# Kernel tuning notes

Hardware: AMD Instinct MI355X
Metric: run time of the kernel (lower is better)

Reference implementation:

```python
import jax, jax.numpy as jnp
import numpy as np

B, IN_C, NHEAD, ATT_C, OUT_C, H, W = 512, 256, 8, 32, 32, 19, 19
EPS = 1e-5


def setup_inputs() -> dict:
    key = jax.random.key(0)
    ks = jax.random.split(key, 4)
    f32 = jnp.float32
    return {
        "x": jax.random.normal(ks[0], (B, IN_C, H, W), f32),
        "Wq": jax.random.normal(ks[1], (NHEAD * ATT_C, IN_C), f32) * 0.05,
        "bq": jnp.zeros((NHEAD * ATT_C,), f32),
        "Wk": jax.random.normal(ks[2], (NHEAD * ATT_C, IN_C), f32) * 0.05,
        "bk": jnp.zeros((NHEAD * ATT_C,), f32),
        "Wv": jax.random.normal(ks[3], (NHEAD * OUT_C, IN_C), f32) * 0.05,
        "bv": jnp.zeros((NHEAD * OUT_C,), f32),
        "gQ": jnp.ones((NHEAD * ATT_C,), f32),
        "betaQ": jnp.zeros((NHEAD * ATT_C,), f32),
        "gK": jnp.ones((NHEAD * ATT_C,), f32),
        "betaK": jnp.zeros((NHEAD * ATT_C,), f32),
        "gV": jnp.ones((NHEAD * OUT_C,), f32),
        "betaV": jnp.zeros((NHEAD * OUT_C,), f32),
    }


def _conv1x1(x, Wt, bt):
    # x: [B,Ci,H,W], Wt: [Co,Ci] -> [B,Co,H,W]
    return jnp.einsum("oi,bihw->bohw", Wt, x) + bt[None, :, None, None]


def _bn(x, g, b):
    # training-mode BatchNorm2d: batch stats over (N,H,W)
    mu = x.mean(axis=(0, 2, 3), keepdims=True)
    var = x.var(axis=(0, 2, 3), keepdims=True)
    return (x - mu) * jax.lax.rsqrt(var + EPS) * g[None, :, None, None] + b[None, :, None, None]


def _neighbors(t):
    # t: [B,C,H,W] -> [B,4,C,H,W] zero-padded 4-neighbor shifts (up,down,left,right)
    p = jnp.pad(t, ((0, 0), (0, 0), (1, 1), (1, 1)))
    return jnp.stack(
        (p[:, :, 0:-2, 1:-1], p[:, :, 2:, 1:-1], p[:, :, 1:-1, 0:-2], p[:, :, 1:-1, 2:]),
        axis=1,
    )


def reference(x, Wq, bq, Wk, bk, Wv, bv, gQ, betaQ, gK, betaK, gV, betaV):
    Q = _bn(_conv1x1(x, Wq, bq), gQ, betaQ)
    K = _bn(_conv1x1(x, Wk, bk), gK, betaK)
    V = _bn(_conv1x1(x, Wv, bv), gV, betaV)

    Kn = _neighbors(K).reshape(B, 4, NHEAD, ATT_C, H, W)
    Q4 = Q.reshape(B, 1, NHEAD, ATT_C, H, W)
    # attention logits: mean over att_c, then * sqrt(att_c)  (usenormmean == 0)
    a = (Q4 * Kn).mean(axis=3) * jnp.float32(ATT_C ** 0.5)  # [B,4,nhead,H,W]
    a = jax.nn.softmax(a, axis=1)[:, :, :, None]  # [B,4,nhead,1,H,W]

    Vn = _neighbors(V).reshape(B, 4, NHEAD, OUT_C, H, W)
    out = (a * Vn).sum(axis=1)  # [B,nhead,out_c,H,W]
    out = out.reshape(B, NHEAD * OUT_C, H, W)
    out = jax.nn.relu(out)  # useRelu == 1
    return out + x  # residual
```

## Files before the change

### kernel.cpp

```cpp
#include <hip/hip_runtime.h>

typedef unsigned short u16;
typedef unsigned int   u32;

#define NB     512
#define NHEADS 8
#define HW     361
#define NPIX   184832
#define NTOT   768
#define EPSBN  1e-5f
#define RS     0.17677669529663687f
#define PSTR   104

typedef __bf16 bf16x8 __attribute__((ext_vector_type(8)));
typedef float  f32x4  __attribute__((ext_vector_type(4)));

__device__ __forceinline__ u16 f2bf(float f) {
  u32 u = __float_as_uint(f);
  u += 0x7fffu + ((u >> 16) & 1u);
  return (u16)(u >> 16);
}
__device__ __forceinline__ float bf2f(u16 v) {
  return __uint_as_float(((u32)v) << 16);
}
__device__ __forceinline__ bf16x8 ldb8(const void* p) {
  return __builtin_bit_cast(bf16x8, *(const uint4*)p);
}
__device__ __forceinline__ float dot2(u32 a, u32 b) {
  return bf2f((u16)a) * bf2f((u16)b) + bf2f((u16)(a >> 16)) * bf2f((u16)(b >> 16));
}
__device__ __forceinline__ float dot8(uint4 a, uint4 b) {
  return dot2(a.x, b.x) + dot2(a.y, b.y) + dot2(a.z, b.z) + dot2(a.w, b.w);
}

__global__ __launch_bounds__(256) void k_prep(
    const float* __restrict__ Wq, const float* __restrict__ bq,
    const float* __restrict__ Wk, const float* __restrict__ bk,
    const float* __restrict__ Wv, const float* __restrict__ bv,
    u16* __restrict__ Wall, float* __restrict__ ball,
    float* __restrict__ sx) {
  const int n = blockIdx.x, t = threadIdx.x;
  const float* src; const float* bs; int r;
  if (n < 256)      { src = Wq; bs = bq; r = n; }
  else if (n < 512) { src = Wk; bs = bk; r = n - 256; }
  else              { src = Wv; bs = bv; r = n - 512; }
  Wall[n * 256 + t] = f2bf(src[r * 256 + t]);
  if (t == 0) ball[n] = bs[r];
  if (n == 0) sx[t] = 0.f;
}

__global__ __launch_bounds__(512) void k_M(
    const float* __restrict__ x, u16* __restrict__ xT,
    float* __restrict__ Mpart, float* __restrict__ sx) {
  __shared__ u16 Als[256 * 64];
  const int tid = threadIdx.x, g = blockIdx.x;
  const int lane = tid & 63, w = tid >> 6;
  const int l15 = lane & 15, kq = lane >> 4;
  const int sc  = tid >> 4;
  const int sq  = tid & 15;
  const int wpx = tid & 63;
  const int wcs = tid >> 6;
  char* Ab = (char*)Als;

  float sxp[8];
  f32x4 acc[2][16];
  #pragma unroll
  for (int i = 0; i < 8; ++i) sxp[i] = 0.f;
  #pragma unroll
  for (int f2 = 0; f2 < 16; ++f2) {
    acc[0][f2] = (f32x4){0.f, 0.f, 0.f, 0.f};
    acc[1][f2] = (f32x4){0.f, 0.f, 0.f, 0.f};
  }

  #pragma unroll 1
  for (int ch = 0; ch < 12; ++ch) {
    const int img = (ch >= 6) ? 1 : 0;
    const int px0 = (ch - img * 6) * 64;
    const int bb  = g * 2 + img;
    const int pb  = px0 + sq * 4;
    #pragma unroll
    for (int i = 0; i < 8; ++i) {
      const int c = sc + 32 * i;
      const float* xp = x + ((size_t)bb * 256 + c) * HW + pb;
      float v0, v1, v2, v3;
      if (pb + 3 < HW) {
        const float4 f4 = *(const float4*)xp;
        v0 = f4.x; v1 = f4.y; v2 = f4.z; v3 = f4.w;
      } else {
        v0 = (pb + 0 < HW) ? xp[0] : 0.f;
        v1 = (pb + 1 < HW) ? xp[1] : 0.f;
        v2 = (pb + 2 < HW) ? xp[2] : 0.f;
        v3 = (pb + 3 < HW) ? xp[3] : 0.f;
      }
      sxp[i] += v0 + v1 + v2 + v3;
      const u32 lo = (u32)f2bf(v0) | ((u32)f2bf(v1) << 16);
      const u32 hi = (u32)f2bf(v2) | ((u32)f2bf(v3) << 16);
      const int slot = (sq >> 1) ^ (c & 7);
      *(uint2*)(Ab + c * 128 + slot * 16 + (sq & 1) * 8) = make_uint2(lo, hi);
    }
    __syncthreads();
    #pragma unroll
    for (int kk = 0; kk < 2; ++kk) {
      const int gl = kk * 4 + kq;
      const int so = ((gl ^ (l15 & 7)) << 4);
      const int r0 = w * 32 + l15;
      const bf16x8 a0 = ldb8(Ab + r0 * 128 + so);
      const bf16x8 a1 = ldb8(Ab + (r0 + 16) * 128 + so);
      #pragma unroll
      for (int f2 = 0; f2 < 16; ++f2) {
        const bf16x8 b = ldb8(Ab + (f2 * 16 + l15) * 128 + so);
        acc[0][f2] = __builtin_amdgcn_mfma_f32_16x16x32_bf16(a0, b, acc[0][f2], 0, 0, 0);
        acc[1][f2] = __builtin_amdgcn_mfma_f32_16x16x32_bf16(a1, b, acc[1][f2], 0, 0, 0);
      }
    }
    const int pxg = px0 + wpx;
    if (pxg < HW) {
      __align__(16) u16 tmp[32];
      #pragma unroll
      for (int j = 0; j < 32; ++j) {
        const int c = wcs * 32 + j;
        tmp[j] = Als[c * 64 + (((wpx >> 3) ^ (c & 7)) << 3) + (wpx & 7)];
      }
      uint4* dst = (uint4*)(xT + ((size_t)bb * HW + pxg) * 256 + wcs * 32);
      dst[0] = ((const uint4*)tmp)[0];
      dst[1] = ((const uint4*)tmp)[1];
      dst[2] = ((const uint4*)tmp)[2];
      dst[3] = ((const uint4*)tmp)[3];
    }
    __syncthreads();
  }
  float* mp = Mpart + (size_t)g * 65536;
  #pragma unroll
  for (int f1 = 0; f1 < 2; ++f1)
    #pragma unroll
    for (int f2 = 0; f2 < 16; ++f2)
      #pragma unroll
      for (int j = 0; j < 4; ++j) {
        const int c1 = w * 32 + f1 * 16 + kq * 4 + j;
        const int c2 = f2 * 16 + l15;
        mp[c1 * 256 + c2] = acc[f1][f2][j];
      }
  #pragma unroll
  for (int i = 0; i < 8; ++i) {
    float v = sxp[i];
    v += __shfl_down(v, 8); v += __shfl_down(v, 4);
    v += __shfl_down(v, 2); v += __shfl_down(v, 1);
    if (sq == 0) atomicAdd(&sx[sc + 32 * i], v);
  }
}

__global__ __launch_bounds__(256) void k_red(const float* __restrict__ Mpart,
                                             float* __restrict__ Mg) {
  const int i = blockIdx.x * 256 + threadIdx.x;
  float s = 0.f;
  #pragma unroll 8
  for (int sl = 0; sl < 256; ++sl) s += Mpart[(size_t)sl * 65536 + i];
  Mg[i] = s;
}

__global__ __launch_bounds__(256) void k_stats2(
    const float* __restrict__ Mg, const float* __restrict__ sx,
    const float* __restrict__ Wq, const float* __restrict__ bq,
    const float* __restrict__ Wk, const float* __restrict__ bk,
    const float* __restrict__ Wv, const float* __restrict__ bv,
    const float* __restrict__ gQ, const float* __restrict__ betaQ,
    const float* __restrict__ gK, const float* __restrict__ betaK,
    const float* __restrict__ gV, const float* __restrict__ betaV,
    float* __restrict__ s_all, float* __restrict__ t_all) {
  __shared__ float ws[256];
  __shared__ float r1[4], r2[4];
  const int n = blockIdx.x, i = threadIdx.x;
  const int which = n >> 8, r = n & 255;
  const float* src = (which == 0) ? Wq : (which == 1) ? Wk : Wv;
  const float wi = src[r * 256 + i];
  ws[i] = wi;
  __syncthreads();
  float colsum = 0.f;
  #pragma unroll 4
  for (int j = 0; j < 256; ++j) colsum += Mg[j * 256 + i] * ws[j];
  float p1 = wi * sx[i];
  float p2 = wi * colsum;
  p1 += __shfl_down(p1, 32); p2 += __shfl_down(p2, 32);
  p1 += __shfl_down(p1, 16); p2 += __shfl_down(p2, 16);
  p1 += __shfl_down(p1, 8);  p2 += __shfl_down(p2, 8);
  p1 += __shfl_down(p1, 4);  p2 += __shfl_down(p2, 4);
  p1 += __shfl_down(p1, 2);  p2 += __shfl_down(p2, 2);
  p1 += __shfl_down(p1, 1);  p2 += __shfl_down(p2, 1);
  const int wv = i >> 6;
  if ((i & 63) == 0) { r1[wv] = p1; r2[wv] = p2; }
  __syncthreads();
  if (i == 0) {
    const float S1 = r1[0] + r1[1] + r1[2] + r1[3];
    const float S2 = r2[0] + r2[1] + r2[2] + r2[3];
    const float* bs = (which == 0) ? bq : (which == 1) ? bk : bv;
    const float* gs = (which == 0) ? gQ : (which == 1) ? gK : gV;
    const float* be = (which == 0) ? betaQ : (which == 1) ? betaK : betaV;
    const float b = bs[r];
    const float P = (float)NPIX;
    const float mean = (S1 + P * b) / P;
    const float Ey2  = (S2 + 2.f * b * S1 + P * b * b) / P;
    const float var  = Ey2 - mean * mean;
    const float s    = gs[r] * rsqrtf(var + EPSBN);
    s_all[n] = s;
    t_all[n] = be[r] - s * mean;
  }
}

__global__ __launch_bounds__(768) void k_fused(
    const u16* __restrict__ xT, const u16* __restrict__ Wall,
    const float* __restrict__ ball,
    const float* __restrict__ s_all, const float* __restrict__ t_all,
    const float* __restrict__ x, float* __restrict__ out) {
  __shared__ u16   Wl[96 * 256];
  __shared__ __align__(16) u16 P[HW * PSTR];
  __shared__ float aL[4 * HW];
  __shared__ float stl[2 * 96];
  const int tid = threadIdx.x;
  const int wg  = blockIdx.x;
  const int bb  = (wg & 7) + 8 * (wg >> 6);
  const int h   = (wg >> 3) & 7;
  const char* Pb = (const char*)P;

  const bool pact = tid < 2 * HW;
  const int  ppx  = pact ? ((tid < HW) ? tid : tid - HW) : 0;
  const int  poc0 = (tid < HW) ? 0 : 16;
  const size_t pgb = ((size_t)bb * 256 + h * 32 + poc0) * HW + ppx;
  float xres[16];
  if (pact) {
    #pragma unroll
    for (int o = 0; o < 16; ++o) xres[o] = x[pgb + (size_t)o * HW];
  }

  if (tid < 96) {
    const int which = tid >> 5, c32 = tid & 31;
    const int n = which * 256 + h * 32 + c32;
    float s = s_all[n];
    float t = s * ball[n] + t_all[n];
    if (tid < 32) { s *= RS; t *= RS; }
    stl[tid] = s; stl[96 + tid] = t;
  }
  #pragma unroll
  for (int i = 0; i < 4; ++i) {
    const int gi = tid + i * 768;
    const int lr = gi >> 5, gg = gi & 31;
    const int which = lr >> 5, c32 = lr & 31;
    uint4 v = *(const uint4*)(Wall + (size_t)(which * 256 + h * 32 + c32) * 256 + gg * 8);
    const int slot = gg ^ (lr & 7);
    *(uint4*)((char*)Wl + lr * 512 + slot * 16) = v;
  }
  __syncthreads();

  const int lane = tid & 63, wv = tid >> 6;
  const int l15 = lane & 15, kq = lane >> 4;
  const u16* xTb = xT + (size_t)bb * HW * 256;

  uint4 bfr[16];
  #pragma unroll
  for (int ks = 0; ks < 8; ++ks) {
    bfr[2 * ks]     = *(const uint4*)(xTb + (size_t)(wv * 32      + l15) * 256 + ks * 32 + kq * 8);
    bfr[2 * ks + 1] = *(const uint4*)(xTb + (size_t)(wv * 32 + 16 + l15) * 256 + ks * 32 + kq * 8);
  }

  f32x4 acc[6][2];
  #pragma unroll
  for (int f = 0; f < 6; ++f) { acc[f][0] = (f32x4){0.f,0.f,0.f,0.f}; acc[f][1] = (f32x4){0.f,0.f,0.f,0.f}; }

  #pragma unroll
  for (int ks = 0; ks < 8; ++ks) {
    bf16x8 b0 = __builtin_bit_cast(bf16x8, bfr[2 * ks]);
    bf16x8 b1 = __builtin_bit_cast(bf16x8, bfr[2 * ks + 1]);
    const int slot = ((ks * 4 + kq) ^ (l15 & 7)) * 16;
    #pragma unroll
    for (int f = 0; f < 6; ++f) {
      const int lr = (f >> 1) * 32 + (f & 1) * 16 + l15;
      bf16x8 a = ldb8((const char*)Wl + lr * 512 + slot);
      acc[f][0] = __builtin_amdgcn_mfma_f32_16x16x32_bf16(a, b0, acc[f][0], 0, 0, 0);
      acc[f][1] = __builtin_amdgcn_mfma_f32_16x16x32_bf16(a, b1, acc[f][1], 0, 0, 0);
    }
  }
  #pragma unroll
  for (int f = 0; f < 6; ++f) {
    #pragma unroll
    for (int j = 0; j < 4; ++j) {
      const int ch = f * 16 + kq * 4 + j;
      const float s = stl[ch], t = stl[96 + ch];
      #pragma unroll
      for (int p2 = 0; p2 < 2; ++p2) {
        const int px = wv * 32 + p2 * 16 + l15;
        if (px < HW) P[px * PSTR + ch] = f2bf(s * acc[f][p2][j] + t);
      }
    }
  }
  __syncthreads();

  if (tid < HW) {
    const int px = tid;
    const int yy = px / 19, xx = px - yy * 19;
    const bool i0 = yy > 0, i1 = yy < 18, i2 = xx > 0, i3 = xx < 18;
    const int pn0 = i0 ? px - 19 : px, pn1 = i1 ? px + 19 : px;
    const int pn2 = i2 ? px - 1  : px, pn3 = i3 ? px + 1  : px;
    const uint4* Qp = (const uint4*)(Pb + px * 208);
    const uint4 q0 = Qp[0], q1 = Qp[1], q2 = Qp[2], q3 = Qp[3];
    const uint4* K0 = (const uint4*)(Pb + pn0 * 208 + 64);
    const uint4* K1 = (const uint4*)(Pb + pn1 * 208 + 64);
    const uint4* K2 = (const uint4*)(Pb + pn2 * 208 + 64);
    const uint4* K3 = (const uint4*)(Pb + pn3 * 208 + 64);
    float l0 = dot8(q0, K0[0]) + dot8(q1, K0[1]) + dot8(q2, K0[2]) + dot8(q3, K0[3]);
    float l1 = dot8(q0, K1[0]) + dot8(q1, K1[1]) + dot8(q2, K1[2]) + dot8(q3, K1[3]);
    float l2 = dot8(q0, K2[0]) + dot8(q1, K2[1]) + dot8(q2, K2[2]) + dot8(q3, K2[3]);
    float l3 = dot8(q0, K3[0]) + dot8(q1, K3[1]) + dot8(q2, K3[2]) + dot8(q3, K3[3]);
    l0 = i0 ? l0 : 0.f; l1 = i1 ? l1 : 0.f;
    l2 = i2 ? l2 : 0.f; l3 = i3 ? l3 : 0.f;
    const float mx = fmaxf(fmaxf(l0, l1), fmaxf(l2, l3));
    const float e0 = __expf(l0 - mx), e1 = __expf(l1 - mx);
    const float e2 = __expf(l2 - mx), e3 = __expf(l3 - mx);
    const float inv = 1.f / (e0 + e1 + e2 + e3);
    aL[0 * HW + px] = i0 ? e0 * inv : 0.f;
    aL[1 * HW + px] = i1 ? e1 * inv : 0.f;
    aL[2 * HW + px] = i2 ? e2 * inv : 0.f;
    aL[3 * HW + px] = i3 ? e3 * inv : 0.f;
  }
  __syncthreads();

  if (pact) {
    const int px = ppx;
    const int yy = px / 19, xx = px - yy * 19;
    const int pn0 = (yy > 0)  ? px - 19 : px, pn1 = (yy < 18) ? px + 19 : px;
    const int pn2 = (xx > 0)  ? px - 1  : px, pn3 = (xx < 18) ? px + 1  : px;
    const float a0 = aL[0 * HW + px], a1 = aL[1 * HW + px];
    const float a2 = aL[2 * HW + px], a3 = aL[3 * HW + px];
    const int vb = 128 + poc0 * 2;
    const uint4* V0 = (const uint4*)(Pb + pn0 * 208 + vb);
    const uint4* V1 = (const uint4*)(Pb + pn1 * 208 + vb);
    const uint4* V2 = (const uint4*)(Pb + pn2 * 208 + vb);
    const uint4* V3 = (const uint4*)(Pb + pn3 * 208 + vb);
    #pragma unroll
    for (int half = 0; half < 2; ++half) {
      const uint4 w0 = V0[half], w1 = V1[half], w2 = V2[half], w3 = V3[half];
      const u32 u0[4] = {w0.x, w0.y, w0.z, w0.w};
      const u32 u1[4] = {w1.x, w1.y, w1.z, w1.w};
      const u32 u2[4] = {w2.x, w2.y, w2.z, w2.w};
      const u32 u3[4] = {w3.x, w3.y, w3.z, w3.w};
      #pragma unroll
      for (int p = 0; p < 4; ++p) {
        const int o = half * 8 + p * 2;
        float vlo = a0 * bf2f((u16)u0[p]) + a1 * bf2f((u16)u1[p])
                  + a2 * bf2f((u16)u2[p]) + a3 * bf2f((u16)u3[p]);
        float vhi = a0 * bf2f((u16)(u0[p] >> 16)) + a1 * bf2f((u16)(u1[p] >> 16))
                  + a2 * bf2f((u16)(u2[p] >> 16)) + a3 * bf2f((u16)(u3[p] >> 16));
        vlo = fmaxf(vlo, 0.f);
        vhi = fmaxf(vhi, 0.f);
        out[pgb + (size_t)o * HW]       = vlo + xres[o];
        out[pgb + (size_t)(o + 1) * HW] = vhi + xres[o + 1];
      }
    }
  }
}

constexpr size_t OFF_XT    = 0;
constexpr size_t SZ_XT     = (size_t)NPIX * 512 + 16384;
constexpr size_t OFF_WALL  = OFF_XT + SZ_XT;
constexpr size_t SZ_WALL   = (size_t)NTOT * 512;
constexpr size_t OFF_BALL  = OFF_WALL + SZ_WALL;
constexpr size_t OFF_M     = OFF_BALL + NTOT * 4;
constexpr size_t SZ_M      = 256 * 256 * 4;
constexpr size_t OFF_SX    = OFF_M + SZ_M;
constexpr size_t OFF_SALL  = OFF_SX + 256 * 4;
constexpr size_t OFF_TALL  = OFF_SALL + NTOT * 4;
constexpr size_t OFF_MPART = OFF_TALL + NTOT * 4;
constexpr size_t SZ_MPART  = (size_t)256 * 65536 * 4;
constexpr size_t WS_NEEDED = OFF_MPART + SZ_MPART;

extern "C" void kernel_launch(void* const* d_in, const int* in_sizes, int n_in,
                              void* d_out, int out_size, void* d_ws, size_t ws_size,
                              hipStream_t stream) {
  (void)in_sizes; (void)n_in; (void)out_size;
  if (ws_size < WS_NEEDED) return;

  const float* x     = (const float*)d_in[0];
  const float* Wq    = (const float*)d_in[1];
  const float* bq    = (const float*)d_in[2];
  const float* Wk    = (const float*)d_in[3];
  const float* bk    = (const float*)d_in[4];
  const float* Wv    = (const float*)d_in[5];
  const float* bv    = (const float*)d_in[6];
  const float* gQ    = (const float*)d_in[7];
  const float* betaQ = (const float*)d_in[8];
  const float* gK    = (const float*)d_in[9];
  const float* betaK = (const float*)d_in[10];
  const float* gV    = (const float*)d_in[11];
  const float* betaV = (const float*)d_in[12];
  float* out = (float*)d_out;

  char* wsp = (char*)d_ws;
  u16*   xT    = (u16*)(wsp + OFF_XT);
  u16*   Wall  = (u16*)(wsp + OFF_WALL);
  float* ball  = (float*)(wsp + OFF_BALL);
  float* Mg    = (float*)(wsp + OFF_M);
  float* sx    = (float*)(wsp + OFF_SX);
  float* s_all = (float*)(wsp + OFF_SALL);
  float* t_all = (float*)(wsp + OFF_TALL);
  float* Mpart = (float*)(wsp + OFF_MPART);

  k_prep<<<NTOT, 256, 0, stream>>>(Wq, bq, Wk, bk, Wv, bv, Wall, ball, sx);
  k_M<<<256, 512, 0, stream>>>(x, xT, Mpart, sx);
  k_red<<<256, 256, 0, stream>>>(Mpart, Mg);
  k_stats2<<<NTOT, 256, 0, stream>>>(Mg, sx, Wq, bq, Wk, bk, Wv, bv,
                                     gQ, betaQ, gK, betaK, gV, betaV, s_all, t_all);
  k_fused<<<NB * NHEADS, 768, 0, stream>>>(xT, Wall, ball, s_all, t_all, x, out);
}
```

Baseline: 401.3 us.

## Process two batch images per fused block with prefetch of next image

Each workgroup of the fused attention kernel now handles two consecutive batch images for one head, so the 96x256 weight slice is loaded into LDS once per two images, and the grid is halved. While the first image's epilogue runs, the second image's xT fragments and residual values are prefetched into registers. The P-tile store is also widened to packed 8-byte writes instead of scalar u16 stores. The cost is higher register pressure from keeping the prefetched operands live, plus half as many blocks to spread across CUs.

Result: faster. 375.9 us (-6.3%).

```diff
diff --git a/kernel.cpp b/kernel.cpp
--- a/kernel.cpp
+++ b/kernel.cpp
@@ -217,20 +217,34 @@
   __shared__ float stl[2 * 96];
   const int tid = threadIdx.x;
   const int wg  = blockIdx.x;
-  const int bb  = (wg & 7) + 8 * (wg >> 6);
-  const int h   = (wg >> 3) & 7;
+  const int xcd = wg & 7, ii = wg >> 3;
+  const int h   = ii & 7;
+  const int pr  = xcd * 32 + (ii >> 3);
+  const int bb0 = pr * 2;
   const char* Pb = (const char*)P;
+
+  const int lane = tid & 63, wv = tid >> 6;
+  const int l15 = lane & 15, kq = lane >> 4;
 
   const bool pact = tid < 2 * HW;
   const int  ppx  = pact ? ((tid < HW) ? tid : tid - HW) : 0;
   const int  poc0 = (tid < HW) ? 0 : 16;
-  const size_t pgb = ((size_t)bb * 256 + h * 32 + poc0) * HW + ppx;
+
+  uint4 bfr[16];
+  {
+    const u16* xTb = xT + (size_t)bb0 * HW * 256;
+    #pragma unroll
+    for (int ks = 0; ks < 8; ++ks) {
+      bfr[2 * ks]     = *(const uint4*)(xTb + (size_t)(wv * 32      + l15) * 256 + ks * 32 + kq * 8);
+      bfr[2 * ks + 1] = *(const uint4*)(xTb + (size_t)(wv * 32 + 16 + l15) * 256 + ks * 32 + kq * 8);
+    }
+  }
   float xres[16];
   if (pact) {
-    #pragma unroll
-    for (int o = 0; o < 16; ++o) xres[o] = x[pgb + (size_t)o * HW];
-  }
-
+    const size_t pg = ((size_t)bb0 * 256 + h * 32 + poc0) * HW + ppx;
+    #pragma unroll
+    for (int o = 0; o < 16; ++o) xres[o] = x[pg + (size_t)o * HW];
+  }
   if (tid < 96) {
     const int which = tid >> 5, c32 = tid & 31;
     const int n = which * 256 + h * 32 + c32;
@@ -250,110 +264,126 @@
   }
   __syncthreads();
 
-  const int lane = tid & 63, wv = tid >> 6;
-  const int l15 = lane & 15, kq = lane >> 4;
-  const u16* xTb = xT + (size_t)bb * HW * 256;
-
-  uint4 bfr[16];
-  #pragma unroll
-  for (int ks = 0; ks < 8; ++ks) {
-    bfr[2 * ks]     = *(const uint4*)(xTb + (size_t)(wv * 32      + l15) * 256 + ks * 32 + kq * 8);
-    bfr[2 * ks + 1] = *(const uint4*)(xTb + (size_t)(wv * 32 + 16 + l15) * 256 + ks * 32 + kq * 8);
-  }
-
-  f32x4 acc[6][2];
-  #pragma unroll
-  for (int f = 0; f < 6; ++f) { acc[f][0] = (f32x4){0.f,0.f,0.f,0.f}; acc[f][1] = (f32x4){0.f,0.f,0.f,0.f}; }
-
-  #pragma unroll
-  for (int ks = 0; ks < 8; ++ks) {
-    bf16x8 b0 = __builtin_bit_cast(bf16x8, bfr[2 * ks]);
-    bf16x8 b1 = __builtin_bit_cast(bf16x8, bfr[2 * ks + 1]);
-    const int slot = ((ks * 4 + kq) ^ (l15 & 7)) * 16;
+  #pragma unroll
+  for (int im = 0; im < 2; ++im) {
+    const int bb = bb0 + im;
+    f32x4 acc[6][2];
     #pragma unroll
     for (int f = 0; f < 6; ++f) {
-      const int lr = (f >> 1) * 32 + (f & 1) * 16 + l15;
-      bf16x8 a = ldb8((const char*)Wl + lr * 512 + slot);
-      acc[f][0] = __builtin_amdgcn_mfma_f32_16x16x32_bf16(a, b0, acc[f][0], 0, 0, 0);
-      acc[f][1] = __builtin_amdgcn_mfma_f32_16x16x32_bf16(a, b1, acc[f][1], 0, 0, 0);
-    }
-  }
-  #pragma unroll
-  for (int f = 0; f < 6; ++f) {
-    #pragma unroll
-    for (int j = 0; j < 4; ++j) {
-      const int ch = f * 16 + kq * 4 + j;
-      const float s = stl[ch], t = stl[96 + ch];
+      acc[f][0] = (f32x4){0.f, 0.f, 0.f, 0.f};
+      acc[f][1] = (f32x4){0.f, 0.f, 0.f, 0.f};
+    }
+    #pragma unroll
+    for (int ks = 0; ks < 8; ++ks) {
+      bf16x8 b0 = __builtin_bit_cast(bf16x8, bfr[2 * ks]);
+      bf16x8 b1 = __builtin_bit_cast(bf16x8, bfr[2 * ks + 1]);
+      const int slot = ((ks * 4 + kq) ^ (l15 & 7)) * 16;
+      #pragma unroll
+      for (int f = 0; f < 6; ++f) {
+        const int lr = (f >> 1) * 32 + (f & 1) * 16 + l15;
+        bf16x8 a = ldb8((const char*)Wl + lr * 512 + slot);
+        acc[f][0] = __builtin_amdgcn_mfma_f32_16x16x32_bf16(a, b0, acc[f][0], 0, 0, 0);
+        acc[f][1] = __builtin_amdgcn_mfma_f32_16x16x32_bf16(a, b1, acc[f][1], 0, 0, 0);
+      }
+    }
+    if (im == 0) {
+      const u16* xTb2 = xT + (size_t)(bb0 + 1) * HW * 256;
+      #pragma unroll
+      for (int ks = 0; ks < 8; ++ks) {
+        bfr[2 * ks]     = *(const uint4*)(xTb2 + (size_t)(wv * 32      + l15) * 256 + ks * 32 + kq * 8);
+        bfr[2 * ks + 1] = *(const uint4*)(xTb2 + (size_t)(wv * 32 + 16 + l15) * 256 + ks * 32 + kq * 8);
+      }
+    }
+    #pragma unroll
+    for (int f = 0; f < 6; ++f) {
+      const int ch0 = f * 16 + kq * 4;
+      const float s0 = stl[ch0], t0 = stl[96 + ch0];
+      const float s1 = stl[ch0 + 1], t1 = stl[96 + ch0 + 1];
+      const float s2 = stl[ch0 + 2], t2 = stl[96 + ch0 + 2];
+      const float s3 = stl[ch0 + 3], t3 = stl[96 + ch0 + 3];
       #pragma unroll
       for (int p2 = 0; p2 < 2; ++p2) {
         const int px = wv * 32 + p2 * 16 + l15;
-        if (px < HW) P[px * PSTR + ch] = f2bf(s * acc[f][p2][j] + t);
-      }
-    }
-  }
-  __syncthreads();
-
-  if (tid < HW) {
-    const int px = tid;
-    const int yy = px / 19, xx = px - yy * 19;
-    const bool i0 = yy > 0, i1 = yy < 18, i2 = xx > 0, i3 = xx < 18;
-    const int pn0 = i0 ? px - 19 : px, pn1 = i1 ? px + 19 : px;
-    const int pn2 = i2 ? px - 1  : px, pn3 = i3 ? px + 1  : px;
-    const uint4* Qp = (const uint4*)(Pb + px * 208);
-    const uint4 q0 = Qp[0], q1 = Qp[1], q2 = Qp[2], q3 = Qp[3];
-    const uint4* K0 = (const uint4*)(Pb + pn0 * 208 + 64);
-    const uint4* K1 = (const uint4*)(Pb + pn1 * 208 + 64);
-    const uint4* K2 = (const uint4*)(Pb + pn2 * 208 + 64);
-    const uint4* K3 = (const uint4*)(Pb + pn3 * 208 + 64);
-    float l0 = dot8(q0, K0[0]) + dot8(q1, K0[1]) + dot8(q2, K0[2]) + dot8(q3, K0[3]);
-    float l1 = dot8(q0, K1[0]) + dot8(q1, K1[1]) + dot8(q2, K1[2]) + dot8(q3, K1[3]);
-    float l2 = dot8(q0, K2[0]) + dot8(q1, K2[1]) + dot8(q2, K2[2]) + dot8(q3, K2[3]);
-    float l3 = dot8(q0, K3[0]) + dot8(q1, K3[1]) + dot8(q2, K3[2]) + dot8(q3, K3[3]);
-    l0 = i0 ? l0 : 0.f; l1 = i1 ? l1 : 0.f;
-    l2 = i2 ? l2 : 0.f; l3 = i3 ? l3 : 0.f;
-    const float mx = fmaxf(fmaxf(l0, l1), fmaxf(l2, l3));
-    const float e0 = __expf(l0 - mx), e1 = __expf(l1 - mx);
-    const float e2 = __expf(l2 - mx), e3 = __expf(l3 - mx);
-    const float inv = 1.f / (e0 + e1 + e2 + e3);
-    aL[0 * HW + px] = i0 ? e0 * inv : 0.f;
-    aL[1 * HW + px] = i1 ? e1 * inv : 0.f;
-    aL[2 * HW + px] = i2 ? e2 * inv : 0.f;
-    aL[3 * HW + px] = i3 ? e3 * inv : 0.f;
-  }
-  __syncthreads();
-
-  if (pact) {
-    const int px = ppx;
-    const int yy = px / 19, xx = px - yy * 19;
-    const int pn0 = (yy > 0)  ? px - 19 : px, pn1 = (yy < 18) ? px + 19 : px;
-    const int pn2 = (xx > 0)  ? px - 1  : px, pn3 = (xx < 18) ? px + 1  : px;
-    const float a0 = aL[0 * HW + px], a1 = aL[1 * HW + px];
-    const float a2 = aL[2 * HW + px], a3 = aL[3 * HW + px];
-    const int vb = 128 + poc0 * 2;
-    const uint4* V0 = (const uint4*)(Pb + pn0 * 208 + vb);
-    const uint4* V1 = (const uint4*)(Pb + pn1 * 208 + vb);
-    const uint4* V2 = (const uint4*)(Pb + pn2 * 208 + vb);
-    const uint4* V3 = (const uint4*)(Pb + pn3 * 208 + vb);
-    #pragma unroll
-    for (int half = 0; half < 2; ++half) {
-      const uint4 w0 = V0[half], w1 = V1[half], w2 = V2[half], w3 = V3[half];
-      const u32 u0[4] = {w0.x, w0.y, w0.z, w0.w};
-      const u32 u1[4] = {w1.x, w1.y, w1.z, w1.w};
-      const u32 u2[4] = {w2.x, w2.y, w2.z, w2.w};
-      const u32 u3[4] = {w3.x, w3.y, w3.z, w3.w};
-      #pragma unroll
-      for (int p = 0; p < 4; ++p) {
-        const int o = half * 8 + p * 2;
-        float vlo = a0 * bf2f((u16)u0[p]) + a1 * bf2f((u16)u1[p])
-                  + a2 * bf2f((u16)u2[p]) + a3 * bf2f((u16)u3[p]);
-        float vhi = a0 * bf2f((u16)(u0[p] >> 16)) + a1 * bf2f((u16)(u1[p] >> 16))
-                  + a2 * bf2f((u16)(u2[p] >> 16)) + a3 * bf2f((u16)(u3[p] >> 16));
-        vlo = fmaxf(vlo, 0.f);
-        vhi = fmaxf(vhi, 0.f);
-        out[pgb + (size_t)o * HW]       = vlo + xres[o];
-        out[pgb + (size_t)(o + 1) * HW] = vhi + xres[o + 1];
-      }
-    }
+        if (px < HW) {
+          const u32 lo = (u32)f2bf(s0 * acc[f][p2][0] + t0)
+                       | ((u32)f2bf(s1 * acc[f][p2][1] + t1) << 16);
+          const u32 hi = (u32)f2bf(s2 * acc[f][p2][2] + t2)
+                       | ((u32)f2bf(s3 * acc[f][p2][3] + t3) << 16);
+          *(uint2*)((char*)P + px * 208 + f * 32 + kq * 8) = make_uint2(lo, hi);
+        }
+      }
+    }
+    __syncthreads();
+
+    if (tid < HW) {
+      const int px = tid;
+      const int yy = px / 19, xx = px - yy * 19;
+      const bool i0 = yy > 0, i1 = yy < 18, i2 = xx > 0, i3 = xx < 18;
+      const int pn0 = i0 ? px - 19 : px, pn1 = i1 ? px + 19 : px;
+      const int pn2 = i2 ? px - 1  : px, pn3 = i3 ? px + 1  : px;
+      const uint4* Qp = (const uint4*)(Pb + px * 208);
+      const uint4 q0 = Qp[0], q1 = Qp[1], q2 = Qp[2], q3 = Qp[3];
+      const uint4* K0 = (const uint4*)(Pb + pn0 * 208 + 64);
+      const uint4* K1 = (const uint4*)(Pb + pn1 * 208 + 64);
+      const uint4* K2 = (const uint4*)(Pb + pn2 * 208 + 64);
+      const uint4* K3 = (const uint4*)(Pb + pn3 * 208 + 64);
+      float l0 = dot8(q0, K0[0]) + dot8(q1, K0[1]) + dot8(q2, K0[2]) + dot8(q3, K0[3]);
+      float l1 = dot8(q0, K1[0]) + dot8(q1, K1[1]) + dot8(q2, K1[2]) + dot8(q3, K1[3]);
+      float l2 = dot8(q0, K2[0]) + dot8(q1, K2[1]) + dot8(q2, K2[2]) + dot8(q3, K2[3]);
+      float l3 = dot8(q0, K3[0]) + dot8(q1, K3[1]) + dot8(q2, K3[2]) + dot8(q3, K3[3]);
+      l0 = i0 ? l0 : 0.f; l1 = i1 ? l1 : 0.f;
+      l2 = i2 ? l2 : 0.f; l3 = i3 ? l3 : 0.f;
+      const float mx = fmaxf(fmaxf(l0, l1), fmaxf(l2, l3));
+      const float e0 = __expf(l0 - mx), e1 = __expf(l1 - mx);
+      const float e2 = __expf(l2 - mx), e3 = __expf(l3 - mx);
+      const float inv = 1.f / (e0 + e1 + e2 + e3);
+      aL[0 * HW + px] = i0 ? e0 * inv : 0.f;
+      aL[1 * HW + px] = i1 ? e1 * inv : 0.f;
+      aL[2 * HW + px] = i2 ? e2 * inv : 0.f;
+      aL[3 * HW + px] = i3 ? e3 * inv : 0.f;
+    }
+    __syncthreads();
+
+    if (pact) {
+      const int px = ppx;
+      const size_t pgb = ((size_t)bb * 256 + h * 32 + poc0) * HW + px;
+      const int yy = px / 19, xx = px - yy * 19;
+      const int pn0 = (yy > 0)  ? px - 19 : px, pn1 = (yy < 18) ? px + 19 : px;
+      const int pn2 = (xx > 0)  ? px - 1  : px, pn3 = (xx < 18) ? px + 1  : px;
+      const float a0 = aL[0 * HW + px], a1 = aL[1 * HW + px];
+      const float a2 = aL[2 * HW + px], a3 = aL[3 * HW + px];
+      const int vb = 128 + poc0 * 2;
+      const uint4* V0 = (const uint4*)(Pb + pn0 * 208 + vb);
+      const uint4* V1 = (const uint4*)(Pb + pn1 * 208 + vb);
+      const uint4* V2 = (const uint4*)(Pb + pn2 * 208 + vb);
+      const uint4* V3 = (const uint4*)(Pb + pn3 * 208 + vb);
+      #pragma unroll
+      for (int half = 0; half < 2; ++half) {
+        const uint4 w0 = V0[half], w1 = V1[half], w2 = V2[half], w3 = V3[half];
+        const u32 u0[4] = {w0.x, w0.y, w0.z, w0.w};
+        const u32 u1[4] = {w1.x, w1.y, w1.z, w1.w};
+        const u32 u2[4] = {w2.x, w2.y, w2.z, w2.w};
+        const u32 u3[4] = {w3.x, w3.y, w3.z, w3.w};
+        #pragma unroll
+        for (int p = 0; p < 4; ++p) {
+          const int o = half * 8 + p * 2;
+          float vlo = a0 * bf2f((u16)u0[p]) + a1 * bf2f((u16)u1[p])
+                    + a2 * bf2f((u16)u2[p]) + a3 * bf2f((u16)u3[p]);
+          float vhi = a0 * bf2f((u16)(u0[p] >> 16)) + a1 * bf2f((u16)(u1[p] >> 16))
+                    + a2 * bf2f((u16)(u2[p] >> 16)) + a3 * bf2f((u16)(u3[p] >> 16));
+          vlo = fmaxf(vlo, 0.f);
+          vhi = fmaxf(vhi, 0.f);
+          out[pgb + (size_t)o * HW]       = vlo + xres[o];
+          out[pgb + (size_t)(o + 1) * HW] = vhi + xres[o + 1];
+        }
+      }
+    }
+    if (im == 0 && pact) {
+      const size_t pg2 = ((size_t)(bb0 + 1) * 256 + h * 32 + poc0) * HW + ppx;
+      #pragma unroll
+      for (int o = 0; o < 16; ++o) xres[o] = x[pg2 + (size_t)o * HW];
+    }
+    __syncthreads();
   }
 }
 
@@ -407,5 +437,5 @@
   k_red<<<256, 256, 0, stream>>>(Mpart, Mg);
   k_stats2<<<NTOT, 256, 0, stream>>>(Mg, sx, Wq, bq, Wk, bk, Wv, bv,
                                      gQ, betaQ, gK, betaK, gV, betaV, s_all, t_all);
-  k_fused<<<NB * NHEADS, 768, 0, stream>>>(xT, Wall, ball, s_all, t_all, x, out);
-}
+  k_fused<<<2048, 768, 0, stream>>>(xT, Wall, ball, s_all, t_all, x, out);
+}
```

## Split fused attention kernel into separate QK-softmax and V-aggregation kernels

Applied to the files above, without the earlier changes.

The single fused kernel, which computed Q, K and V projections, softmax and the weighted sum in one block, becomes two kernels. One computes Q/K and the softmax weights and writes them to a global buffer. The other recomputes the V projection and applies those weights with ReLU and the residual. The aim is to shrink LDS use and register pressure per block for better occupancy, and the split also adds an XOR-swizzled LDS layout with packed stores. The cost is a second pass over xT, an extra global round trip for the attention weights, and one more launch.

Result: slower. 418.9 us (+4.4%).

```diff
diff --git a/kernel.cpp b/kernel.cpp
--- a/kernel.cpp
+++ b/kernel.cpp
@@ -10,7 +10,6 @@
 #define NTOT   768
 #define EPSBN  1e-5f
 #define RS     0.17677669529663687f
-#define PSTR   104
 
 typedef __bf16 bf16x8 __attribute__((ext_vector_type(8)));
 typedef float  f32x4  __attribute__((ext_vector_type(4)));
@@ -206,47 +205,36 @@
   }
 }
 
-__global__ __launch_bounds__(768) void k_fused(
+__global__ __launch_bounds__(768) void k_qk(
     const u16* __restrict__ xT, const u16* __restrict__ Wall,
     const float* __restrict__ ball,
     const float* __restrict__ s_all, const float* __restrict__ t_all,
-    const float* __restrict__ x, float* __restrict__ out) {
-  __shared__ u16   Wl[96 * 256];
-  __shared__ __align__(16) u16 P[HW * PSTR];
-  __shared__ float aL[4 * HW];
-  __shared__ float stl[2 * 96];
-  const int tid = threadIdx.x;
-  const int wg  = blockIdx.x;
-  const int bb  = (wg & 7) + 8 * (wg >> 6);
-  const int h   = (wg >> 3) & 7;
-  const char* Pb = (const char*)P;
-
-  const bool pact = tid < 2 * HW;
-  const int  ppx  = pact ? ((tid < HW) ? tid : tid - HW) : 0;
-  const int  poc0 = (tid < HW) ? 0 : 16;
-  const size_t pgb = ((size_t)bb * 256 + h * 32 + poc0) * HW + ppx;
-  float xres[16];
-  if (pact) {
-    #pragma unroll
-    for (int o = 0; o < 16; ++o) xres[o] = x[pgb + (size_t)o * HW];
-  }
-
-  if (tid < 96) {
+    float* __restrict__ aL4) {
+  __shared__ u16 Wqk[64 * 256];
+  __shared__ __align__(16) u16 Pq[HW * 64];
+  __shared__ float stl[2 * 64];
+  const int tid = threadIdx.x, wg = blockIdx.x;
+  const int xcd = wg & 7, rest = wg >> 3;
+  const int h = rest & 7, bb = xcd + 8 * (rest >> 3);
+  const char* Pb = (const char*)Pq;
+
+  if (tid < 64) {
     const int which = tid >> 5, c32 = tid & 31;
     const int n = which * 256 + h * 32 + c32;
     float s = s_all[n];
     float t = s * ball[n] + t_all[n];
-    if (tid < 32) { s *= RS; t *= RS; }
-    stl[tid] = s; stl[96 + tid] = t;
-  }
-  #pragma unroll
-  for (int i = 0; i < 4; ++i) {
+    if (which == 0) { s *= RS; t *= RS; }
+    stl[tid] = s; stl[64 + tid] = t;
+  }
+  #pragma unroll
+  for (int i = 0; i < 3; ++i) {
     const int gi = tid + i * 768;
-    const int lr = gi >> 5, gg = gi & 31;
-    const int which = lr >> 5, c32 = lr & 31;
-    uint4 v = *(const uint4*)(Wall + (size_t)(which * 256 + h * 32 + c32) * 256 + gg * 8);
-    const int slot = gg ^ (lr & 7);
-    *(uint4*)((char*)Wl + lr * 512 + slot * 16) = v;
+    if (gi < 2048) {
+      const int lr = gi >> 5, gg = gi & 31;
+      const int n = ((lr < 32) ? 0 : 256) + h * 32 + (lr & 31);
+      uint4 v = *(const uint4*)(Wall + (size_t)n * 256 + gg * 8);
+      *(uint4*)((char*)Wqk + lr * 512 + (gg ^ (lr & 7)) * 16) = v;
+    }
   }
   __syncthreads();
 
@@ -254,40 +242,52 @@
   const int l15 = lane & 15, kq = lane >> 4;
   const u16* xTb = xT + (size_t)bb * HW * 256;
 
-  uint4 bfr[16];
-  #pragma unroll
-  for (int ks = 0; ks < 8; ++ks) {
-    bfr[2 * ks]     = *(const uint4*)(xTb + (size_t)(wv * 32      + l15) * 256 + ks * 32 + kq * 8);
-    bfr[2 * ks + 1] = *(const uint4*)(xTb + (size_t)(wv * 32 + 16 + l15) * 256 + ks * 32 + kq * 8);
-  }
-
-  f32x4 acc[6][2];
-  #pragma unroll
-  for (int f = 0; f < 6; ++f) { acc[f][0] = (f32x4){0.f,0.f,0.f,0.f}; acc[f][1] = (f32x4){0.f,0.f,0.f,0.f}; }
-
-  #pragma unroll
-  for (int ks = 0; ks < 8; ++ks) {
-    bf16x8 b0 = __builtin_bit_cast(bf16x8, bfr[2 * ks]);
-    bf16x8 b1 = __builtin_bit_cast(bf16x8, bfr[2 * ks + 1]);
-    const int slot = ((ks * 4 + kq) ^ (l15 & 7)) * 16;
-    #pragma unroll
-    for (int f = 0; f < 6; ++f) {
-      const int lr = (f >> 1) * 32 + (f & 1) * 16 + l15;
-      bf16x8 a = ldb8((const char*)Wl + lr * 512 + slot);
-      acc[f][0] = __builtin_amdgcn_mfma_f32_16x16x32_bf16(a, b0, acc[f][0], 0, 0, 0);
-      acc[f][1] = __builtin_amdgcn_mfma_f32_16x16x32_bf16(a, b1, acc[f][1], 0, 0, 0);
-    }
-  }
-  #pragma unroll
-  for (int f = 0; f < 6; ++f) {
-    #pragma unroll
-    for (int j = 0; j < 4; ++j) {
-      const int ch = f * 16 + kq * 4 + j;
-      const float s = stl[ch], t = stl[96 + ch];
+  f32x4 acc[4][2];
+  #pragma unroll
+  for (int f = 0; f < 4; ++f) {
+    acc[f][0] = (f32x4){0.f, 0.f, 0.f, 0.f};
+    acc[f][1] = (f32x4){0.f, 0.f, 0.f, 0.f};
+  }
+  #pragma unroll
+  for (int kb = 0; kb < 4; ++kb) {
+    uint4 bfr[4];
+    #pragma unroll
+    for (int j = 0; j < 2; ++j) {
+      const int ks = kb * 2 + j;
+      bfr[j * 2]     = *(const uint4*)(xTb + (size_t)(wv * 32      + l15) * 256 + ks * 32 + kq * 8);
+      bfr[j * 2 + 1] = *(const uint4*)(xTb + (size_t)(wv * 32 + 16 + l15) * 256 + ks * 32 + kq * 8);
+    }
+    #pragma unroll
+    for (int j = 0; j < 2; ++j) {
+      const int ks = kb * 2 + j;
+      const bf16x8 b0 = __builtin_bit_cast(bf16x8, bfr[j * 2]);
+      const bf16x8 b1 = __builtin_bit_cast(bf16x8, bfr[j * 2 + 1]);
+      const int slot = ((ks * 4 + kq) ^ (l15 & 7)) * 16;
       #pragma unroll
-      for (int p2 = 0; p2 < 2; ++p2) {
-        const int px = wv * 32 + p2 * 16 + l15;
-        if (px < HW) P[px * PSTR + ch] = f2bf(s * acc[f][p2][j] + t);
+      for (int f = 0; f < 4; ++f) {
+        const bf16x8 a = ldb8((const char*)Wqk + (f * 16 + l15) * 512 + slot);
+        acc[f][0] = __builtin_amdgcn_mfma_f32_16x16x32_bf16(a, b0, acc[f][0], 0, 0, 0);
+        acc[f][1] = __builtin_amdgcn_mfma_f32_16x16x32_bf16(a, b1, acc[f][1], 0, 0, 0);
+      }
+    }
+  }
+  #pragma unroll
+  for (int f = 0; f < 4; ++f) {
+    const int ch0 = f * 16 + kq * 4;
+    const float s0 = stl[ch0],     t0 = stl[64 + ch0];
+    const float s1 = stl[ch0 + 1], t1 = stl[64 + ch0 + 1];
+    const float s2 = stl[ch0 + 2], t2 = stl[64 + ch0 + 2];
+    const float s3 = stl[ch0 + 3], t3 = stl[64 + ch0 + 3];
+    #pragma unroll
+    for (int p2 = 0; p2 < 2; ++p2) {
+      const int px = wv * 32 + p2 * 16 + l15;
+      if (px < HW) {
+        const u32 lo = (u32)f2bf(s0 * acc[f][p2][0] + t0)
+                     | ((u32)f2bf(s1 * acc[f][p2][1] + t1) << 16);
+        const u32 hi = (u32)f2bf(s2 * acc[f][p2][2] + t2)
+                     | ((u32)f2bf(s3 * acc[f][p2][3] + t3) << 16);
+        const int slot = (2 * f + (kq >> 1)) ^ (px & 7);
+        *(uint2*)((char*)Pq + px * 128 + slot * 16 + (kq & 1) * 8) = make_uint2(lo, hi);
       }
     }
   }
@@ -299,26 +299,128 @@
     const bool i0 = yy > 0, i1 = yy < 18, i2 = xx > 0, i3 = xx < 18;
     const int pn0 = i0 ? px - 19 : px, pn1 = i1 ? px + 19 : px;
     const int pn2 = i2 ? px - 1  : px, pn3 = i3 ? px + 1  : px;
-    const uint4* Qp = (const uint4*)(Pb + px * 208);
-    const uint4 q0 = Qp[0], q1 = Qp[1], q2 = Qp[2], q3 = Qp[3];
-    const uint4* K0 = (const uint4*)(Pb + pn0 * 208 + 64);
-    const uint4* K1 = (const uint4*)(Pb + pn1 * 208 + 64);
-    const uint4* K2 = (const uint4*)(Pb + pn2 * 208 + 64);
-    const uint4* K3 = (const uint4*)(Pb + pn3 * 208 + 64);
-    float l0 = dot8(q0, K0[0]) + dot8(q1, K0[1]) + dot8(q2, K0[2]) + dot8(q3, K0[3]);
-    float l1 = dot8(q0, K1[0]) + dot8(q1, K1[1]) + dot8(q2, K1[2]) + dot8(q3, K1[3]);
-    float l2 = dot8(q0, K2[0]) + dot8(q1, K2[1]) + dot8(q2, K2[2]) + dot8(q3, K2[3]);
-    float l3 = dot8(q0, K3[0]) + dot8(q1, K3[1]) + dot8(q2, K3[2]) + dot8(q3, K3[3]);
+    uint4 q[4], k0[4], k1[4], k2[4], k3[4];
+    #pragma unroll
+    for (int g = 0; g < 4; ++g) {
+      q[g]  = *(const uint4*)(Pb + px  * 128 + ((g ^ (px  & 7)) * 16));
+      k0[g] = *(const uint4*)(Pb + pn0 * 128 + (((4 + g) ^ (pn0 & 7)) * 16));
+      k1[g] = *(const uint4*)(Pb + pn1 * 128 + (((4 + g) ^ (pn1 & 7)) * 16));
+      k2[g] = *(const uint4*)(Pb + pn2 * 128 + (((4 + g) ^ (pn2 & 7)) * 16));
+      k3[g] = *(const uint4*)(Pb + pn3 * 128 + (((4 + g) ^ (pn3 & 7)) * 16));
+    }
+    float l0 = 0.f, l1 = 0.f, l2 = 0.f, l3 = 0.f;
+    #pragma unroll
+    for (int g = 0; g < 4; ++g) {
+      l0 += dot8(q[g], k0[g]); l1 += dot8(q[g], k1[g]);
+      l2 += dot8(q[g], k2[g]); l3 += dot8(q[g], k3[g]);
+    }
     l0 = i0 ? l0 : 0.f; l1 = i1 ? l1 : 0.f;
     l2 = i2 ? l2 : 0.f; l3 = i3 ? l3 : 0.f;
     const float mx = fmaxf(fmaxf(l0, l1), fmaxf(l2, l3));
     const float e0 = __expf(l0 - mx), e1 = __expf(l1 - mx);
     const float e2 = __expf(l2 - mx), e3 = __expf(l3 - mx);
     const float inv = 1.f / (e0 + e1 + e2 + e3);
-    aL[0 * HW + px] = i0 ? e0 * inv : 0.f;
-    aL[1 * HW + px] = i1 ? e1 * inv : 0.f;
-    aL[2 * HW + px] = i2 ? e2 * inv : 0.f;
-    aL[3 * HW + px] = i3 ? e3 * inv : 0.f;
+    float4 av;
+    av.x = i0 ? e0 * inv : 0.f;
+    av.y = i1 ? e1 * inv : 0.f;
+    av.z = i2 ? e2 * inv : 0.f;
+    av.w = i3 ? e3 * inv : 0.f;
+    *(float4*)&aL4[(((size_t)(bb * NHEADS + h) * HW) + px) * 4] = av;
+  }
+}
+
+__global__ __launch_bounds__(768) void k_v(
+    const u16* __restrict__ xT, const u16* __restrict__ Wall,
+    const float* __restrict__ ball,
+    const float* __restrict__ s_all, const float* __restrict__ t_all,
+    const float* __restrict__ aL4, const float* __restrict__ x,
+    float* __restrict__ out) {
+  __shared__ u16 Wv[32 * 256];
+  __shared__ __align__(16) u16 Pv[HW * 40];
+  __shared__ float stl[2 * 32];
+  const int tid = threadIdx.x, wg = blockIdx.x;
+  const int xcd = wg & 7, rest = wg >> 3;
+  const int h = rest & 7, bb = xcd + 8 * (rest >> 3);
+  const char* Pb = (const char*)Pv;
+
+  const bool pact = tid < 2 * HW;
+  const int  ppx  = pact ? ((tid < HW) ? tid : tid - HW) : 0;
+  const int  poc0 = (tid < HW) ? 0 : 16;
+  const size_t pgb = ((size_t)bb * 256 + h * 32 + poc0) * HW + ppx;
+  float xres[16];
+  float4 aw = make_float4(0.f, 0.f, 0.f, 0.f);
+  if (pact) {
+    aw = *(const float4*)&aL4[(((size_t)(bb * NHEADS + h) * HW) + ppx) * 4];
+    #pragma unroll
+    for (int o = 0; o < 16; ++o) xres[o] = x[pgb + (size_t)o * HW];
+  }
+
+  if (tid < 32) {
+    const int n = 512 + h * 32 + tid;
+    const float s = s_all[n];
+    stl[tid] = s; stl[32 + tid] = s * ball[n] + t_all[n];
+  }
+  #pragma unroll
+  for (int i = 0; i < 2; ++i) {
+    const int gi = tid + i * 768;
+    if (gi < 1024) {
+      const int lr = gi >> 5, gg = gi & 31;
+      const int n = 512 + h * 32 + lr;
+      uint4 v = *(const uint4*)(Wall + (size_t)n * 256 + gg * 8);
+      *(uint4*)((char*)Wv + lr * 512 + (gg ^ (lr & 7)) * 16) = v;
+    }
+  }
+  __syncthreads();
+
+  const int lane = tid & 63, wv = tid >> 6;
+  const int l15 = lane & 15, kq = lane >> 4;
+  const u16* xTb = xT + (size_t)bb * HW * 256;
+
+  f32x4 acc[2][2];
+  acc[0][0] = (f32x4){0.f,0.f,0.f,0.f}; acc[0][1] = (f32x4){0.f,0.f,0.f,0.f};
+  acc[1][0] = (f32x4){0.f,0.f,0.f,0.f}; acc[1][1] = (f32x4){0.f,0.f,0.f,0.f};
+  #pragma unroll
+  for (int kb = 0; kb < 4; ++kb) {
+    uint4 bfr[4];
+    #pragma unroll
+    for (int j = 0; j < 2; ++j) {
+      const int ks = kb * 2 + j;
+      bfr[j * 2]     = *(const uint4*)(xTb + (size_t)(wv * 32      + l15) * 256 + ks * 32 + kq * 8);
+      bfr[j * 2 + 1] = *(const uint4*)(xTb + (size_t)(wv * 32 + 16 + l15) * 256 + ks * 32 + kq * 8);
+    }
+    #pragma unroll
+    for (int j = 0; j < 2; ++j) {
+      const int ks = kb * 2 + j;
+      const bf16x8 b0 = __builtin_bit_cast(bf16x8, bfr[j * 2]);
+      const bf16x8 b1 = __builtin_bit_cast(bf16x8, bfr[j * 2 + 1]);
+      const int slot = ((ks * 4 + kq) ^ (l15 & 7)) * 16;
+      #pragma unroll
+      for (int f = 0; f < 2; ++f) {
+        const bf16x8 a = ldb8((const char*)Wv + (f * 16 + l15) * 512 + slot);
+        acc[f][0] = __builtin_amdgcn_mfma_f32_16x16x32_bf16(a, b0, acc[f][0], 0, 0, 0);
+        acc[f][1] = __builtin_amdgcn_mfma_f32_16x16x32_bf16(a, b1, acc[f][1], 0, 0, 0);
+      }
+    }
+  }
+  #pragma unroll
+  for (int f = 0; f < 2; ++f) {
+    const int ch0 = f * 16 + kq * 4;
+    const float s0 = stl[ch0],     t0 = stl[32 + ch0];
+    const float s1 = stl[ch0 + 1], t1 = stl[32 + ch0 + 1];
+    const float s2 = stl[ch0 + 2], t2 = stl[32 + ch0 + 2];
+    const float s3 = stl[ch0 + 3], t3 = stl[32 + ch0 + 3];
+    #pragma unroll
+    for (int p2 = 0; p2 < 2; ++p2) {
+      const int px = wv * 32 + p2 * 16 + l15;
+      if (px < HW) {
+        const u32 lo = (u32)f2bf(s0 * acc[f][p2][0] + t0)
+                     | ((u32)f2bf(s1 * acc[f][p2][1] + t1) << 16);
+        const u32 hi = (u32)f2bf(s2 * acc[f][p2][2] + t2)
+                     | ((u32)f2bf(s3 * acc[f][p2][3] + t3) << 16);
+        *(uint2*)((char*)Pv + px * 80 + (2 * f + (kq >> 1)) * 16 + (kq & 1) * 8)
+            = make_uint2(lo, hi);
+      }
+    }
   }
   __syncthreads();
 
@@ -327,16 +429,14 @@
     const int yy = px / 19, xx = px - yy * 19;
     const int pn0 = (yy > 0)  ? px - 19 : px, pn1 = (yy < 18) ? px + 19 : px;
     const int pn2 = (xx > 0)  ? px - 1  : px, pn3 = (xx < 18) ? px + 1  : px;
-    const float a0 = aL[0 * HW + px], a1 = aL[1 * HW + px];
-    const float a2 = aL[2 * HW + px], a3 = aL[3 * HW + px];
-    const int vb = 128 + poc0 * 2;
-    const uint4* V0 = (const uint4*)(Pb + pn0 * 208 + vb);
-    const uint4* V1 = (const uint4*)(Pb + pn1 * 208 + vb);
-    const uint4* V2 = (const uint4*)(Pb + pn2 * 208 + vb);
-    const uint4* V3 = (const uint4*)(Pb + pn3 * 208 + vb);
+    const float a0 = aw.x, a1 = aw.y, a2 = aw.z, a3 = aw.w;
+    const int gb = (poc0 >> 3) * 16;
     #pragma unroll
     for (int half = 0; half < 2; ++half) {
-      const uint4 w0 = V0[half], w1 = V1[half], w2 = V2[half], w3 = V3[half];
+      const uint4 w0 = *(const uint4*)(Pb + pn0 * 80 + gb + half * 16);
+      const uint4 w1 = *(const uint4*)(Pb + pn1 * 80 + gb + half * 16);
+      const uint4 w2 = *(const uint4*)(Pb + pn2 * 80 + gb + half * 16);
+      const uint4 w3 = *(const uint4*)(Pb + pn3 * 80 + gb + half * 16);
       const u32 u0[4] = {w0.x, w0.y, w0.z, w0.w};
       const u32 u1[4] = {w1.x, w1.y, w1.z, w1.w};
       const u32 u2[4] = {w2.x, w2.y, w2.z, w2.w};
@@ -367,7 +467,9 @@
 constexpr size_t OFF_SX    = OFF_M + SZ_M;
 constexpr size_t OFF_SALL  = OFF_SX + 256 * 4;
 constexpr size_t OFF_TALL  = OFF_SALL + NTOT * 4;
-constexpr size_t OFF_MPART = OFF_TALL + NTOT * 4;
+constexpr size_t OFF_AL4   = OFF_TALL + NTOT * 4;
+constexpr size_t SZ_AL4    = (size_t)NB * NHEADS * HW * 16;
+constexpr size_t OFF_MPART = OFF_AL4 + SZ_AL4;
 constexpr size_t SZ_MPART  = (size_t)256 * 65536 * 4;
 constexpr size_t WS_NEEDED = OFF_MPART + SZ_MPART;
 
@@ -400,6 +502,7 @@
   float* sx    = (float*)(wsp + OFF_SX);
   float* s_all = (float*)(wsp + OFF_SALL);
   float* t_all = (float*)(wsp + OFF_TALL);
+  float* aL4   = (float*)(wsp + OFF_AL4);
   float* Mpart = (float*)(wsp + OFF_MPART);
 
   k_prep<<<NTOT, 256, 0, stream>>>(Wq, bq, Wk, bk, Wv, bv, Wall, ball, sx);
@@ -407,5 +510,6 @@
   k_red<<<256, 256, 0, stream>>>(Mpart, Mg);
   k_stats2<<<NTOT, 256, 0, stream>>>(Mg, sx, Wq, bq, Wk, bk, Wv, bv,
                                      gQ, betaQ, gK, betaK, gV, betaV, s_all, t_all);
-  k_fused<<<NB * NHEADS, 768, 0, stream>>>(xT, Wall, ball, s_all, t_all, x, out);
-}
+  k_qk<<<NB * NHEADS, 768, 0, stream>>>(xT, Wall, ball, s_all, t_all, aL4);
+  k_v<<<NB * NHEADS, 768, 0, stream>>>(xT, Wall, ball, s_all, t_all, aL4, x, out);
+}
```
